# Performance work log

Hardware: AMD Instinct MI355X
Metric: run time of the kernel (lower is better)

The kernel has to match this reference:

```python
import jax, jax.numpy as jnp
import numpy as np
from functools import partial

HIDDEN = 1024
NT = 4096


def setup_inputs() -> dict:
    key = jax.random.key(0)
    k1, k2, k3, k4 = jax.random.split(key, 4)
    # PyTorch nn.Linear default init ~ U(-1/sqrt(fan_in), 1/sqrt(fan_in)); use small
    # normal weights for numerical stability over 4096 recurrent steps.
    W1 = jax.random.normal(k1, (1, HIDDEN), dtype=jnp.float32) * 0.05
    b1 = jax.random.normal(k2, (HIDDEN,), dtype=jnp.float32) * 0.05
    W2 = jax.random.normal(k3, (HIDDEN, 1), dtype=jnp.float32) * 0.05
    b2 = jax.random.normal(k4, (1,), dtype=jnp.float32) * 0.05
    x0 = jnp.ones((1,), dtype=jnp.float32)            # x_m[0:1] in source
    dt = jnp.full((1,), 2.0 / (NT - 1), dtype=jnp.float32)  # linspace(0,2,nt) spacing
    return {"x0": x0, "dt": dt, "nt": NT, "W1": W1, "b1": b1, "W2": W2, "b2": b2}


def reference(x0, dt, nt, W1, b1, W2, b2):
    dt_s = dt[0]

    def nn(x):  # x: [1] -> [1]; Linear(1,H) -> ReLU -> Linear(H,1)
        h = jnp.maximum(x @ W1 + b1, 0.0)  # [H]
        return h @ W2 + b2                  # [1]

    def step(x_k, _):
        x_next = x_k + dt_s * nn(x_k)
        return x_next, x_next

    _, outs = jax.lax.scan(step, x0, None, length=nt - 1)  # outs: [nt-1, 1]
    x_pred = jnp.concatenate([x0, outs[:, 0]])             # [nt]
    return x_pred
```

## Files before the change

### kernel.cpp

```cpp
#include <hip/hip_runtime.h>
#include <math.h>

#define UPL 16
#define NTH 512
#define MAXRUNS 512

#define DPPMV(v, ctrl) __int_as_float(__builtin_amdgcn_update_dpp( \
    __float_as_int(v), __float_as_int(v), (ctrl), 0xf, 0xf, false))

__device__ inline float wave_min64(float v) {
    v = fminf(v, DPPMV(v, 0x111));
    v = fminf(v, DPPMV(v, 0x112));
    v = fminf(v, DPPMV(v, 0x114));
    v = fminf(v, DPPMV(v, 0x118));
    v = fminf(v, DPPMV(v, 0x142));
    v = fminf(v, DPPMV(v, 0x143));
    return __int_as_float(__builtin_amdgcn_readlane(__float_as_int(v), 63));
}
__device__ inline float wave_max64(float v) {
    v = fmaxf(v, DPPMV(v, 0x111));
    v = fmaxf(v, DPPMV(v, 0x112));
    v = fmaxf(v, DPPMV(v, 0x114));
    v = fmaxf(v, DPPMV(v, 0x118));
    v = fmaxf(v, DPPMV(v, 0x142));
    v = fmaxf(v, DPPMV(v, 0x143));
    return __int_as_float(__builtin_amdgcn_readlane(__float_as_int(v), 63));
}

template<int CTRL>
__device__ inline double ddpp0(double v) {
    long long l = __double_as_longlong(v);
    int lo = __builtin_amdgcn_update_dpp(0, (int)(l & 0xffffffffLL), CTRL, 0xf, 0xf, true);
    int hi = __builtin_amdgcn_update_dpp(0, (int)(l >> 32),          CTRL, 0xf, 0xf, true);
    return __longlong_as_double(((long long)hi << 32) | (unsigned long long)(unsigned)lo);
}
__device__ inline double wave_dsum64(double v) {
    v += ddpp0<0x111>(v);
    v += ddpp0<0x112>(v);
    v += ddpp0<0x114>(v);
    v += ddpp0<0x118>(v);
    v += ddpp0<0x142>(v);
    v += ddpp0<0x143>(v);
    long long l = __double_as_longlong(v);
    int lo = __builtin_amdgcn_readlane((int)(l & 0xffffffffLL), 63);
    int hi = __builtin_amdgcn_readlane((int)(l >> 32), 63);
    return __longlong_as_double(((long long)hi << 32) | (unsigned long long)(unsigned)lo);
}

__device__ inline double geo_val(double xs, double delta, double L2, double m) {
    double t = m * L2;
    if (fabs(t) < 0.043) {
        double e = t * 0.6931471805599453094;
        double g = e * (1.0 + e * (0.5 + e * (1.0/6.0 + e * (1.0/24.0 + e * (1.0/120.0 + e * (1.0/720.0))))));
        return (xs + delta) + delta * g;
    }
    return xs + delta * (double)exp2f((float)t);
}
__device__ inline double lin_val(double xst, double d, double m) { return fma(m, d, xst); }

__global__ __launch_bounds__(NTH) void euler_kernel(
    const float* __restrict__ x0p, const float* __restrict__ dtp,
    const float* __restrict__ W1, const float* __restrict__ b1,
    const float* __restrict__ W2, const float* __restrict__ b2p,
    float* __restrict__ out, int nt)
{
    __shared__ int    s_k0[MAXRUNS];
    __shared__ double s_p0[MAXRUNS], s_p1[MAXRUNS], s_p2[MAXRUNS];
    __shared__ unsigned char s_ln[MAXRUNS];
    __shared__ int s_nr, s_fe;

    const int tid = threadIdx.x;
    const float x0f = x0p[0];
    const float INFF = __builtin_huge_valf();

    if (tid < 64) {
        const int lane = tid;
        const float dtf = dtp[0], b2 = b2p[0];

        float tk[UPL], da[UPL], dc[UPL];
        double accA = 0.0, accB = 0.0;
        const float4* W14 = (const float4*)W1;
        const float4* B14 = (const float4*)b1;
        const float4* W24 = (const float4*)W2;
        #pragma unroll
        for (int i = 0; i < UPL / 4; ++i) {
            float4 w1v = W14[i * 64 + lane];
            float4 b1v = B14[i * 64 + lane];
            float4 w2v = W24[i * 64 + lane];
            float w1a[4] = {w1v.x, w1v.y, w1v.z, w1v.w};
            float b1a[4] = {b1v.x, b1v.y, b1v.z, b1v.w};
            float w2a[4] = {w2v.x, w2v.y, w2v.z, w2v.w};
            #pragma unroll
            for (int j = 0; j < 4; ++j) {
                int idx = i * 4 + j;
                float w1 = w1a[j], bb = b1a[j], w2 = w2a[j];
                float a = w1 * w2, cc = bb * w2;
                float key, d_a, d_c;
                if (w1 > 0.0f)      { key = -bb / w1; d_a =  a; d_c =  cc; }
                else if (w1 < 0.0f) { key = -bb / w1; d_a = -a; d_c = -cc; accA += (double)a; accB += (double)cc; }
                else                { key = INFF;     d_a = 0.0f; d_c = 0.0f; accB += (double)(fmaxf(bb, 0.0f) * w2); }
                tk[idx] = key; da[idx] = d_a; dc[idx] = d_c;
                if (key <= x0f) { accA += (double)d_a; accB += (double)d_c; }
            }
        }
        double A = wave_dsum64(accA);
        double B = wave_dsum64(accB) + (double)b2;

        const double dt = (double)dtf;
        double x = (double)x0f;
        float  xf = x0f;
        int k = 0, r = 0, fend = 0;
        const int last = nt - 1;

        while (k < last && r < MAXRUNS) {
            double eps = dt * A, d = dt * B;
            double v = eps * x + d;
            int remaining = last - k;
            int m, lin; double P0, P1, P2;

            if (v == 0.0) { lin = 1; P0 = x; P1 = 0.0; P2 = 0.0; m = remaining; }
            else {
                const bool up = (v > 0.0);
                float T;
                if (up) {
                    float q0 = INFF, q1 = INFF, q2 = INFF, q3 = INFF;
                    #pragma unroll
                    for (int i = 0; i < UPL; i += 4) {
                        q0 = fminf(q0, (tk[i    ] > xf) ? tk[i    ] : INFF);
                        q1 = fminf(q1, (tk[i + 1] > xf) ? tk[i + 1] : INFF);
                        q2 = fminf(q2, (tk[i + 2] > xf) ? tk[i + 2] : INFF);
                        q3 = fminf(q3, (tk[i + 3] > xf) ? tk[i + 3] : INFF);
                    }
                    T = wave_min64(fminf(fminf(q0, q1), fminf(q2, q3)));
                } else {
                    float q0 = -INFF, q1 = -INFF, q2 = -INFF, q3 = -INFF;
                    #pragma unroll
                    for (int i = 0; i < UPL; i += 4) {
                        q0 = fmaxf(q0, (tk[i    ] < xf) ? tk[i    ] : -INFF);
                        q1 = fmaxf(q1, (tk[i + 1] < xf) ? tk[i + 1] : -INFF);
                        q2 = fmaxf(q2, (tk[i + 2] < xf) ? tk[i + 2] : -INFF);
                        q3 = fmaxf(q3, (tk[i + 3] < xf) ? tk[i + 3] : -INFF);
                    }
                    T = wave_max64(fmaxf(fmaxf(q0, q1), fmaxf(q2, q3)));
                }
                const double Td = (double)T;

                if (eps == 0.0) {
                    lin = 1; P0 = x; P1 = d; P2 = 0.0;
                    if (isinf(T)) m = remaining;
                    else {
                        double mm = (Td - x) / d;
                        m = (mm < (double)remaining) ? ((mm < 1.0) ? 1 : (int)ceil(mm)) : remaining;
                        int g = 0;
                        while (m < remaining && g++ < 8) { double y = lin_val(P0, P1, (double)m);     if (up ? (y >= Td) : (y <= Td)) break; ++m; }
                        g = 0;
                        while (m > 1 && g++ < 8)         { double y = lin_val(P0, P1, (double)(m-1)); if (up ? (y >= Td) : (y <= Td)) --m; else break; }
                    }
                } else {
                    lin = 0;
                    double r0 = (double)__builtin_amdgcn_rcpf((float)eps);
                    r0 = r0 * (2.0 - eps * r0);
                    r0 = r0 * (2.0 - eps * r0);
                    double xs = -d * r0;
                    double delta = x - xs;
                    double L2 = eps * (1.0 - eps * (0.5 - eps * (1.0/3.0 - eps * 0.25)))
                              * 1.4426950408889634074;
                    P0 = xs; P1 = delta; P2 = L2;
                    if (isinf(T)) m = remaining;
                    else {
                        float uf  = (float)(Td - x) * __builtin_amdgcn_rcpf((float)delta);
                        float mmf = __log2f(1.0f + uf) / (float)L2;
                        if (!(mmf < (float)remaining + 8.0f)) m = remaining;
                        else {
                            float msf = mmf - 8.0f;
                            int mstart = (msf > 1.0f) ? (int)msf : 1;
                            m = 0;
                            bool firstTry = true;
                            #pragma unroll 1
                            for (int t = 0; t < 8 && m == 0; ++t) {
                                if (mstart >= remaining) { m = remaining; break; }
                                double y = geo_val(P0, P1, P2, (double)(mstart + lane));
                                bool crossed = up ? (y >= Td) : (y <= Td);
                                unsigned long long cm = __ballot(crossed);
                                if (cm) {
                                    int idx = __ffsll(cm) - 1;
                                    if (idx == 0 && mstart > 1 && firstTry) {
                                        mstart = (mstart > 64) ? (mstart - 64) : 1;
                                        firstTry = false;
                                        continue;
                                    }
                                    int mcf = mstart + idx;
                                    m = (mcf < remaining) ? mcf : remaining;
                                } else {
                                    mstart += 64;
                                    firstTry = false;
                                }
                            }
                            if (m == 0) m = remaining;
                        }
                    }
                }
            }

            if (lane == 0) {
                s_k0[r] = k; s_ln[r] = (unsigned char)lin;
                s_p0[r] = P0; s_p1[r] = P1; s_p2[r] = P2;
            }
            ++r;
            double xn = lin ? lin_val(P0, P1, (double)m) : geo_val(P0, P1, P2, (double)m);
            k += m; fend = k;
            float xnf = (float)xn;

            if (k < last) {
                float sA = 0.0f, sB = 0.0f; int cnt = 0;
                bool upm = (xnf > xf);
                #pragma unroll
                for (int i = 0; i < UPL; ++i) {
                    float tv = tk[i];
                    bool in = upm ? (tv > xf && tv <= xnf) : (tv > xnf && tv <= xf);
                    if (in) { sA += da[i]; sB += dc[i]; ++cnt; }
                }
                unsigned long long msk = __ballot(cnt > 0);
                double dsA = 0.0, dsB = 0.0;
                while (msk) {
                    int l = __ffsll(msk) - 1;
                    msk &= (msk - 1);
                    dsA += (double)__shfl(sA, l);
                    dsB += (double)__shfl(sB, l);
                }
                if (upm) { A += dsA; B += dsB; } else { A -= dsA; B -= dsB; }
            }
            x = xn; xf = xnf;
        }

        while (k < last) {
            double eps = dt * A, d = dt * B;
            double xn = x + (eps * x + d);
            ++k;
            if (lane == 0) out[k] = (float)xn;
            float xnf = (float)xn;
            float sA = 0.0f, sB = 0.0f;
            bool upm = (xnf > xf);
            #pragma unroll
            for (int i = 0; i < UPL; ++i) {
                float tv = tk[i];
                bool in = upm ? (tv > xf && tv <= xnf) : (tv > xnf && tv <= xf);
                if (in) { sA += da[i]; sB += dc[i]; }
            }
            #pragma unroll
            for (int off = 32; off; off >>= 1) {
                sA += __shfl_xor(sA, off);
                sB += __shfl_xor(sB, off);
            }
            if (upm) { A += (double)sA; B += (double)sB; }
            else     { A -= (double)sA; B -= (double)sB; }
            x = xn; xf = xnf;
        }

        if (lane == 0) { s_nr = r; s_fe = fend; }
    }
    __syncthreads();

    {
        const int nr = s_nr, fe = s_fe;
        for (int kk = tid; kk <= fe; kk += NTH) {
            if (kk == 0) { out[0] = x0f; continue; }
            int lo = 0, hi = nr - 1;
            while (lo < hi) {
                int mid = (lo + hi + 1) >> 1;
                if (s_k0[mid] < kk) lo = mid; else hi = mid - 1;
            }
            double m = (double)(kk - s_k0[lo]);
            double vv = s_ln[lo] ? lin_val(s_p0[lo], s_p1[lo], m)
                                 : geo_val(s_p0[lo], s_p1[lo], s_p2[lo], m);
            out[kk] = (float)vv;
        }
    }
}

extern "C" void kernel_launch(void* const* d_in, const int* in_sizes, int n_in,
                              void* d_out, int out_size, void* d_ws, size_t ws_size,
                              hipStream_t stream) {
    const float* x0 = (const float*)d_in[0];
    const float* dt = (const float*)d_in[1];
    const float* W1 = (const float*)d_in[3];
    const float* b1 = (const float*)d_in[4];
    const float* W2 = (const float*)d_in[5];
    const float* b2 = (const float*)d_in[6];
    float* out = (float*)d_out;
    const int nt = out_size;
    euler_kernel<<<1, NTH, 0, stream>>>(x0, dt, W1, b1, W2, b2, out, nt);
}
```

Baseline: 29.68 us.

## Compute run crossing step analytically and fuse next-breakpoint search into update loop

After: 25.67 us. 1.16x faster.

```diff
diff --git a/kernel.cpp b/kernel.cpp
--- a/kernel.cpp
+++ b/kernel.cpp
@@ -4,6 +4,7 @@
 #define UPL 16
 #define NTH 512
 #define MAXRUNS 512
+#define LOG2E 1.4426950408889634074
 
 #define DPPMV(v, ctrl) __int_as_float(__builtin_amdgcn_update_dpp( \
     __float_as_int(v), __float_as_int(v), (ctrl), 0xf, 0xf, false))
@@ -45,6 +46,13 @@
     int lo = __builtin_amdgcn_readlane((int)(l & 0xffffffffLL), 63);
     int hi = __builtin_amdgcn_readlane((int)(l >> 32), 63);
     return __longlong_as_double(((long long)hi << 32) | (unsigned long long)(unsigned)lo);
+}
+
+__device__ inline double nrecip(double v) {
+    double r = (double)__builtin_amdgcn_rcpf((float)v);
+    r = r * (2.0 - v * r);
+    r = r * (2.0 - v * r);
+    return r;
 }
 
 __device__ inline double geo_val(double xs, double delta, double L2, double m) {
@@ -112,92 +120,77 @@
         int k = 0, r = 0, fend = 0;
         const int last = nt - 1;
 
+        float T_up, T_dn;
+        {
+            float nu = INFF, nd = -INFF;
+            #pragma unroll
+            for (int i = 0; i < UPL; ++i) {
+                float tv = tk[i];
+                nu = fminf(nu, (tv > xf) ? tv : INFF);
+                nd = fmaxf(nd, (tv < xf) ? tv : -INFF);
+            }
+            T_up = wave_min64(nu);
+            T_dn = wave_max64(nd);
+        }
+
         while (k < last && r < MAXRUNS) {
             double eps = dt * A, d = dt * B;
             double v = eps * x + d;
             int remaining = last - k;
-            int m, lin; double P0, P1, P2;
-
-            if (v == 0.0) { lin = 1; P0 = x; P1 = 0.0; P2 = 0.0; m = remaining; }
-            else {
+            int m, lin; double P0, P1, P2, xn;
+
+            if (v == 0.0) {
+                lin = 1; P0 = x; P1 = 0.0; P2 = 0.0; m = remaining; xn = x;
+            } else {
                 const bool up = (v > 0.0);
-                float T;
-                if (up) {
-                    float q0 = INFF, q1 = INFF, q2 = INFF, q3 = INFF;
-                    #pragma unroll
-                    for (int i = 0; i < UPL; i += 4) {
-                        q0 = fminf(q0, (tk[i    ] > xf) ? tk[i    ] : INFF);
-                        q1 = fminf(q1, (tk[i + 1] > xf) ? tk[i + 1] : INFF);
-                        q2 = fminf(q2, (tk[i + 2] > xf) ? tk[i + 2] : INFF);
-                        q3 = fminf(q3, (tk[i + 3] > xf) ? tk[i + 3] : INFF);
-                    }
-                    T = wave_min64(fminf(fminf(q0, q1), fminf(q2, q3)));
-                } else {
-                    float q0 = -INFF, q1 = -INFF, q2 = -INFF, q3 = -INFF;
-                    #pragma unroll
-                    for (int i = 0; i < UPL; i += 4) {
-                        q0 = fmaxf(q0, (tk[i    ] < xf) ? tk[i    ] : -INFF);
-                        q1 = fmaxf(q1, (tk[i + 1] < xf) ? tk[i + 1] : -INFF);
-                        q2 = fmaxf(q2, (tk[i + 2] < xf) ? tk[i + 2] : -INFF);
-                        q3 = fmaxf(q3, (tk[i + 3] < xf) ? tk[i + 3] : -INFF);
-                    }
-                    T = wave_max64(fmaxf(fmaxf(q0, q1), fmaxf(q2, q3)));
-                }
+                const float T = up ? T_up : T_dn;
                 const double Td = (double)T;
 
                 if (eps == 0.0) {
                     lin = 1; P0 = x; P1 = d; P2 = 0.0;
                     if (isinf(T)) m = remaining;
                     else {
-                        double mm = (Td - x) / d;
+                        double mm = (Td - x) * nrecip(d);
                         m = (mm < (double)remaining) ? ((mm < 1.0) ? 1 : (int)ceil(mm)) : remaining;
                         int g = 0;
                         while (m < remaining && g++ < 8) { double y = lin_val(P0, P1, (double)m);     if (up ? (y >= Td) : (y <= Td)) break; ++m; }
                         g = 0;
                         while (m > 1 && g++ < 8)         { double y = lin_val(P0, P1, (double)(m-1)); if (up ? (y >= Td) : (y <= Td)) --m; else break; }
                     }
+                    xn = lin_val(P0, P1, (double)m);
                 } else {
                     lin = 0;
-                    double r0 = (double)__builtin_amdgcn_rcpf((float)eps);
-                    r0 = r0 * (2.0 - eps * r0);
-                    r0 = r0 * (2.0 - eps * r0);
-                    double xs = -d * r0;
+                    double xs = -d * nrecip(eps);
                     double delta = x - xs;
-                    double L2 = eps * (1.0 - eps * (0.5 - eps * (1.0/3.0 - eps * 0.25)))
-                              * 1.4426950408889634074;
+                    double Ln = eps * (1.0 - eps * (0.5 - eps * (1.0/3.0 - eps * 0.25)));
+                    double L2 = Ln * LOG2E;
                     P0 = xs; P1 = delta; P2 = L2;
-                    if (isinf(T)) m = remaining;
-                    else {
-                        float uf  = (float)(Td - x) * __builtin_amdgcn_rcpf((float)delta);
-                        float mmf = __log2f(1.0f + uf) / (float)L2;
-                        if (!(mmf < (float)remaining + 8.0f)) m = remaining;
+
+                    if (isinf(T)) {
+                        m = remaining;
+                        xn = geo_val(P0, P1, P2, (double)m);
+                    } else {
+                        double u = (Td - x) * nrecip(delta);
+                        bool exits = (eps > 0.0) ? true : (u > -1.0 && u < 0.0);
+                        if (!exits) m = remaining;
                         else {
-                            float msf = mmf - 8.0f;
-                            int mstart = (msf > 1.0f) ? (int)msf : 1;
-                            m = 0;
-                            bool firstTry = true;
-                            #pragma unroll 1
-                            for (int t = 0; t < 8 && m == 0; ++t) {
-                                if (mstart >= remaining) { m = remaining; break; }
-                                double y = geo_val(P0, P1, P2, (double)(mstart + lane));
-                                bool crossed = up ? (y >= Td) : (y <= Td);
-                                unsigned long long cm = __ballot(crossed);
-                                if (cm) {
-                                    int idx = __ffsll(cm) - 1;
-                                    if (idx == 0 && mstart > 1 && firstTry) {
-                                        mstart = (mstart > 64) ? (mstart - 64) : 1;
-                                        firstTry = false;
-                                        continue;
-                                    }
-                                    int mcf = mstart + idx;
-                                    m = (mcf < remaining) ? mcf : remaining;
-                                } else {
-                                    mstart += 64;
-                                    firstTry = false;
-                                }
-                            }
-                            if (m == 0) m = remaining;
+                            double lrn = (fabs(u) <= 0.25)
+                                ? u * (1.0 - u * (0.5 - u * (1.0/3.0 - u * (0.25 - u * (0.2 - u * (1.0/6.0))))))
+                                : log(1.0 + u);
+                            double mm = lrn * nrecip(Ln);
+                            m = (mm < (double)remaining) ? ((mm < 1.0) ? 1 : (int)ceil(mm)) : remaining;
                         }
+                        double ym = geo_val(P0, P1, P2, (double)m);
+                        double yp = geo_val(P0, P1, P2, (double)(m - 1));
+                        int g = 0;
+                        while (m < remaining && g++ < 8 && !(up ? (ym >= Td) : (ym <= Td))) {
+                            ++m; yp = ym; ym = geo_val(P0, P1, P2, (double)m);
+                        }
+                        g = 0;
+                        while (m > 1 && g++ < 8 && (up ? (yp >= Td) : (yp <= Td))) {
+                            --m; ym = yp; yp = geo_val(P0, P1, P2, (double)(m - 1));
+                        }
+                        xn = ym;
                     }
                 }
             }
@@ -207,19 +200,23 @@
                 s_p0[r] = P0; s_p1[r] = P1; s_p2[r] = P2;
             }
             ++r;
-            double xn = lin ? lin_val(P0, P1, (double)m) : geo_val(P0, P1, P2, (double)m);
             k += m; fend = k;
             float xnf = (float)xn;
 
             if (k < last) {
                 float sA = 0.0f, sB = 0.0f; int cnt = 0;
+                float nu = INFF, nd = -INFF;
                 bool upm = (xnf > xf);
                 #pragma unroll
                 for (int i = 0; i < UPL; ++i) {
                     float tv = tk[i];
                     bool in = upm ? (tv > xf && tv <= xnf) : (tv > xnf && tv <= xf);
                     if (in) { sA += da[i]; sB += dc[i]; ++cnt; }
+                    nu = fminf(nu, (tv > xnf) ? tv : INFF);
+                    nd = fmaxf(nd, (tv < xnf) ? tv : -INFF);
                 }
+                T_up = wave_min64(nu);
+                T_dn = wave_max64(nd);
                 unsigned long long msk = __ballot(cnt > 0);
                 double dsA = 0.0, dsB = 0.0;
                 while (msk) {
```
